# Optimization experiments

Hardware: AMD Instinct MI355X
Metric: run time of the kernel (lower is better)

The kernel has to match this reference:

```python
import jax, jax.numpy as jnp
import numpy as np

S = 4096
F = 512  # in_features, head_num == 1 so per-head dim == F


def setup_inputs() -> dict:
    key = jax.random.key(0)
    ks = jax.random.split(key, 11)
    std = 0.02
    inp = {
        "q": jax.random.normal(ks[0], (1, S, F), jnp.float32),
        "k": jax.random.normal(ks[1], (1, S, F), jnp.float32),
        "v": jax.random.normal(ks[2], (1, S, F), jnp.float32),
        "Wq": jax.random.normal(ks[3], (F, F), jnp.float32) * std,
        "bq": jax.random.normal(ks[4], (F,), jnp.float32) * std,
        "Wk": jax.random.normal(ks[5], (F, F), jnp.float32) * std,
        "bk": jax.random.normal(ks[6], (F,), jnp.float32) * std,
        "Wv": jax.random.normal(ks[7], (F, F), jnp.float32) * std,
        "bv": jax.random.normal(ks[8], (F,), jnp.float32) * std,
        "Wo": jax.random.normal(ks[9], (F, F), jnp.float32) * std,
        "bo": jax.random.normal(ks[10], (F,), jnp.float32) * std,
    }
    return inp


def reference(q, k, v, Wq, bq, Wk, bk, Wv, bv, Wo, bo):
    dk = Wq.shape[0]  # head_num == 1 -> per-head dim equals in_features
    # q_k, q_v: projections of q WITHOUT activation (as in original forward)
    q_k = q @ Wk.T + bk            # (1, S, F)
    q_v = q @ Wv.T + bv            # (1, S, F)
    # activated projections (F.relu)
    qq = jax.nn.relu(q @ Wq.T + bq)[0]  # (S, F)
    kk = jax.nn.relu(k @ Wk.T + bk)[0]  # (S, F)
    vv = jax.nn.relu(v @ Wv.T + bv)[0]  # (S, F)
    # diagonal of qq @ q_k^T, computed without materializing the SxS matrix
    q_att = jnp.sum(qq * q_k[0], axis=-1, keepdims=True)  # (S, 1)
    scores = jnp.einsum('sd,td->st', qq, kk)               # (S, S)
    scores = jnp.concatenate([scores, q_att], axis=-1)     # (S, S+1)
    scores = scores / np.sqrt(dk + 1).astype(np.float32)
    attn = jax.nn.softmax(scores, axis=-1)                 # (S, S+1)
    res = attn[:, :-1] @ vv                                # (S, F)
    res = q_v[0] * q_att + res                             # elementwise fusion
    y = res[None]                                          # (1, S, F)
    y = jax.nn.relu(y @ Wo.T + bo)
    return y
```

## Files before the change

kernel.cpp:

```cpp
#include <hip/hip_runtime.h>
#include <math.h>

#define S_LEN 4096
#define F_DIM 512
#define PSPLIT 8
#define FIXED_M 4.0f

typedef __attribute__((ext_vector_type(8))) short bf16x8;
typedef __attribute__((ext_vector_type(4))) float f32x4;

__device__ __forceinline__ unsigned short f2bf(float x) {
    union { float f; unsigned u; } v; v.f = x;
    unsigned r = v.u + 0x7fffu + ((v.u >> 16) & 1u);
    return (unsigned short)(r >> 16);
}
__device__ __forceinline__ float bf2f(unsigned short b) {
    union { unsigned u; float f; } v; v.u = ((unsigned)b) << 16;
    return v.f;
}
__device__ __forceinline__ void load_lds16(const void* g, void* l) {
    __builtin_amdgcn_global_load_lds(
        (const __attribute__((address_space(1))) unsigned int*)g,
        (__attribute__((address_space(3))) unsigned int*)l, 16, 0, 0);
}

struct CastArgs {
    const float* src[7];
    unsigned short* dst[7];
    int n4[7];
};
__global__ void cast_all(CastArgs a) {
    int r = blockIdx.y;
    int i = blockIdx.x * blockDim.x + threadIdx.x;
    if (i >= a.n4[r]) return;
    float4 v = ((const float4*)a.src[r])[i];
    ushort4 o;
    o.x = f2bf(v.x); o.y = f2bf(v.y); o.z = f2bf(v.z); o.w = f2bf(v.w);
    ((ushort4*)a.dst[r])[i] = o;
}

__global__ void transpose_bf16(const unsigned short* __restrict__ src,
                               unsigned short* __restrict__ dst) {
    __shared__ __align__(16) unsigned short tile[64][72];
    const int s0 = blockIdx.x * 64, f0 = blockIdx.y * 64;
    const int tid = threadIdx.x;
#pragma unroll
    for (int it = 0; it < 2; ++it) {
        int u = it * 256 + tid;
        int r = u >> 3, c = (u & 7) * 8;
        *(uint4*)&tile[r][c] = *(const uint4*)(src + (size_t)(s0 + r) * F_DIM + f0 + c);
    }
    __syncthreads();
#pragma unroll
    for (int it = 0; it < 2; ++it) {
        int u = it * 256 + tid;
        int fl = u >> 3, sc = (u & 7) * 8;
        unsigned short tmp[8];
#pragma unroll
        for (int i = 0; i < 8; ++i) tmp[i] = tile[sc + i][fl];
        *(uint4*)(dst + (size_t)(f0 + fl) * S_LEN + s0 + sc) = *(uint4*)tmp;
    }
}

#define GEMM_KLOOP(XPTR, LDX, WPTR, LDW, KBEG, KEND)                                  \
    for (int k0 = (KBEG); k0 < (KEND); k0 += 64) {                                    \
        __syncthreads();                                                              \
        _Pragma("unroll")                                                             \
        for (int i = 0; i < 2; ++i) {                                                 \
            int c = w * 2 + i;                                                        \
            _Pragma("unroll")                                                         \
            for (int kh = 0; kh < 2; ++kh) {                                          \
                load_lds16((XPTR) + (size_t)(m0 + c * 16 + ln) * (LDX) + k0 + kh * 32 + quad * 8, \
                           &As[(c * 2 + kh) * 512]);                                  \
                load_lds16((WPTR) + (size_t)(n0 + c * 16 + ln) * (LDW) + k0 + kh * 32 + quad * 8, \
                           &Bs[(c * 2 + kh) * 512]);                                  \
            }                                                                         \
        }                                                                             \
        __syncthreads();                                                              \
        _Pragma("unroll")                                                             \
        for (int kh = 0; kh < 2; ++kh) {                                              \
            bf16x8 af[4], bfr[4];                                                     \
            _Pragma("unroll")                                                         \
            for (int mt = 0; mt < 4; ++mt)                                            \
                af[mt] = *(const bf16x8*)&As[((wr * 4 + mt) * 2 + kh) * 512 + l * 8];  \
            _Pragma("unroll")                                                         \
            for (int nt = 0; nt < 4; ++nt)                                            \
                bfr[nt] = *(const bf16x8*)&Bs[((wc * 4 + nt) * 2 + kh) * 512 + l * 8]; \
            _Pragma("unroll")                                                         \
            for (int mt = 0; mt < 4; ++mt)                                            \
                _Pragma("unroll")                                                     \
                for (int nt = 0; nt < 4; ++nt)                                        \
                    acc[mt][nt] = __builtin_amdgcn_mfma_f32_16x16x32_bf16(            \
                        af[mt], bfr[nt], acc[mt][nt], 0, 0, 0);                       \
        }                                                                             \
    }

struct GemmDesc {
    const unsigned short* X;
    const unsigned short* W;
    const float* bias;
    unsigned short* out_bf;
    float* out_f32;
    int relu;
};
struct GemmArgs { GemmDesc d[5]; };

__launch_bounds__(256, 2)
__global__ void gemm128(GemmArgs args) {
    __shared__ __align__(16) unsigned short As[16 * 512];
    __shared__ __align__(16) unsigned short Bs[16 * 512];
    const GemmDesc d = args.d[blockIdx.y >> 2];
    const int n0 = (blockIdx.y & 3) * 128;
    const int m0 = blockIdx.x * 128;
    const int tid = threadIdx.x;
    const int w = tid >> 6, l = tid & 63, quad = l >> 4, ln = l & 15;
    const int wr = w >> 1, wc = w & 1;

    f32x4 acc[4][4];
    f32x4 zero4 = {0.f, 0.f, 0.f, 0.f};
#pragma unroll
    for (int i = 0; i < 4; ++i)
#pragma unroll
        for (int j = 0; j < 4; ++j) acc[i][j] = zero4;

    GEMM_KLOOP(d.X, F_DIM, d.W, F_DIM, 0, F_DIM)

#pragma unroll
    for (int mt = 0; mt < 4; ++mt)
#pragma unroll
        for (int nt = 0; nt < 4; ++nt)
#pragma unroll
            for (int r = 0; r < 4; ++r) {
                int row = m0 + wr * 64 + mt * 16 + quad * 4 + r;
                int col = n0 + wc * 64 + nt * 16 + ln;
                float vv = acc[mt][nt][r] + d.bias[col];
                if (d.relu) vv = fmaxf(vv, 0.f);
                if (d.out_bf)  d.out_bf[(size_t)row * F_DIM + col] = f2bf(vv);
                if (d.out_f32) d.out_f32[(size_t)row * F_DIM + col] = vv;
            }
}

__launch_bounds__(256, 2)
__global__ void gemm_exp(const unsigned short* __restrict__ X,
                         const unsigned short* __restrict__ W,
                         unsigned short* __restrict__ P,
                         float* __restrict__ lpart) {
    __shared__ __align__(16) unsigned short As[16 * 512];
    __shared__ __align__(16) unsigned short Bs[16 * 512];
    __shared__ float lsum[2][2][64];
    const float scale = 0.04415108f;
    const int nb = blockIdx.y;
    const int n0 = nb * 128;
    const int m0 = blockIdx.x * 128;
    const int tid = threadIdx.x;
    const int w = tid >> 6, l = tid & 63, quad = l >> 4, ln = l & 15;
    const int wr = w >> 1, wc = w & 1;

    f32x4 acc[4][4];
    f32x4 zero4 = {0.f, 0.f, 0.f, 0.f};
#pragma unroll
    for (int i = 0; i < 4; ++i)
#pragma unroll
        for (int j = 0; j < 4; ++j) acc[i][j] = zero4;

    GEMM_KLOOP(X, F_DIM, W, F_DIM, 0, F_DIM)

    float rs[4][4];
#pragma unroll
    for (int mt = 0; mt < 4; ++mt)
#pragma unroll
        for (int r = 0; r < 4; ++r) rs[mt][r] = 0.f;

#pragma unroll
    for (int mt = 0; mt < 4; ++mt)
#pragma unroll
        for (int nt = 0; nt < 4; ++nt)
#pragma unroll
            for (int r = 0; r < 4; ++r) {
                int row = m0 + wr * 64 + mt * 16 + quad * 4 + r;
                int col = n0 + wc * 64 + nt * 16 + ln;
                float p = __expf(acc[mt][nt][r] * scale - FIXED_M);
                P[(size_t)row * S_LEN + col] = f2bf(p);
                rs[mt][r] += p;
            }
#pragma unroll
    for (int mt = 0; mt < 4; ++mt)
#pragma unroll
        for (int r = 0; r < 4; ++r) {
            float v = rs[mt][r];
            v += __shfl_xor(v, 1);
            v += __shfl_xor(v, 2);
            v += __shfl_xor(v, 4);
            v += __shfl_xor(v, 8);
            if (ln == 0) lsum[wr][wc][mt * 16 + quad * 4 + r] = v;
        }
    __syncthreads();
    if (tid < 128)
        lpart[(size_t)nb * S_LEN + m0 + tid] =
            lsum[tid >> 6][0][tid & 63] + lsum[tid >> 6][1][tid & 63];
}

__launch_bounds__(256, 2)
__global__ void gemm_pv(const unsigned short* __restrict__ P,
                        const unsigned short* __restrict__ vt,
                        unsigned short* __restrict__ O_p) {
    __shared__ __align__(16) unsigned short As[16 * 512];
    __shared__ __align__(16) unsigned short Bs[16 * 512];
    const int nb = blockIdx.y & 3;
    const int split = blockIdx.y >> 2;
    const int n0 = nb * 128;
    const int m0 = blockIdx.x * 128;
    const int koff = split * (S_LEN / PSPLIT);
    const int tid = threadIdx.x;
    const int w = tid >> 6, l = tid & 63, quad = l >> 4, ln = l & 15;
    const int wr = w >> 1, wc = w & 1;

    f32x4 acc[4][4];
    f32x4 zero4 = {0.f, 0.f, 0.f, 0.f};
#pragma unroll
    for (int i = 0; i < 4; ++i)
#pragma unroll
        for (int j = 0; j < 4; ++j) acc[i][j] = zero4;

    GEMM_KLOOP(P, S_LEN, vt, S_LEN, koff, koff + S_LEN / PSPLIT)

    unsigned short* Op = O_p + (size_t)split * S_LEN * F_DIM;
#pragma unroll
    for (int mt = 0; mt < 4; ++mt)
#pragma unroll
        for (int nt = 0; nt < 4; ++nt)
#pragma unroll
            for (int r = 0; r < 4; ++r) {
                int row = m0 + wr * 64 + mt * 16 + quad * 4 + r;
                int col = n0 + wc * 64 + nt * 16 + ln;
                Op[(size_t)row * F_DIM + col] = f2bf(acc[mt][nt][r]);
            }
}

__global__ void combine_kernel(const unsigned short* __restrict__ O_p,
                               const float* __restrict__ lpart,
                               const unsigned short* __restrict__ qq,
                               const unsigned short* __restrict__ qk,
                               const unsigned short* __restrict__ qv,
                               unsigned short* __restrict__ res_bf) {
    const float scale = 0.04415108f;
    int row = blockIdx.x;
    int t = threadIdx.x;
    int wv = t >> 6, l = t & 63;
    __shared__ float wsum[2];

    ushort4 a = *(const ushort4*)(qq + (size_t)row * F_DIM + t * 4);
    ushort4 b = *(const ushort4*)(qk + (size_t)row * F_DIM + t * 4);
    float part = bf2f(a.x) * bf2f(b.x) + bf2f(a.y) * bf2f(b.y) +
                 bf2f(a.z) * bf2f(b.z) + bf2f(a.w) * bf2f(b.w);
#pragma unroll
    for (int off = 32; off >= 1; off >>= 1) part += __shfl_xor(part, off);
    if (l == 0) wsum[wv] = part;
    __syncthreads();
    float qa = wsum[0] + wsum[1];

    float denom = __expf(qa * scale - FIXED_M);
#pragma unroll
    for (int i = 0; i < 32; ++i) denom += lpart[(size_t)i * S_LEN + row];
    float inv = 1.f / denom;

    for (int f = t; f < F_DIM; f += 128) {
        float acc = 0.f;
#pragma unroll
        for (int i = 0; i < PSPLIT; ++i)
            acc += bf2f(O_p[((size_t)i * S_LEN + row) * F_DIM + f]);
        float r = bf2f(qv[(size_t)row * F_DIM + f]) * qa + acc * inv;
        res_bf[(size_t)row * F_DIM + f] = f2bf(r);
    }
}

extern "C" void kernel_launch(void* const* d_in, const int* in_sizes, int n_in,
                              void* d_out, int out_size, void* d_ws, size_t ws_size,
                              hipStream_t stream) {
    const float* q  = (const float*)d_in[0];
    const float* k  = (const float*)d_in[1];
    const float* v  = (const float*)d_in[2];
    const float* Wq = (const float*)d_in[3];
    const float* bq = (const float*)d_in[4];
    const float* Wk = (const float*)d_in[5];
    const float* bk = (const float*)d_in[6];
    const float* Wv = (const float*)d_in[7];
    const float* bv = (const float*)d_in[8];
    const float* Wo = (const float*)d_in[9];
    const float* bo = (const float*)d_in[10];
    float* out = (float*)d_out;

    char* p = (char*)d_ws;
    auto alloc = [&](size_t bytes) -> char* {
        char* r = p; p += (bytes + 255) & ~(size_t)255; return r;
    };
    const size_t SF = (size_t)S_LEN * F_DIM;
    unsigned short* q_bf  = (unsigned short*)alloc(SF * 2);
    unsigned short* k_bf  = (unsigned short*)alloc(SF * 2);
    unsigned short* v_bf  = (unsigned short*)alloc(SF * 2);
    unsigned short* qq_bf = (unsigned short*)alloc(SF * 2);
    unsigned short* kk_bf = (unsigned short*)alloc(SF * 2);
    unsigned short* vv_bf = (unsigned short*)alloc(SF * 2);
    unsigned short* vt_bf = (unsigned short*)alloc(SF * 2);
    unsigned short* qk_bf = (unsigned short*)alloc(SF * 2);
    unsigned short* qv_bf = (unsigned short*)alloc(SF * 2);
    unsigned short* res_bf = (unsigned short*)alloc(SF * 2);
    unsigned short* wq_bf = (unsigned short*)alloc((size_t)F_DIM * F_DIM * 2);
    unsigned short* wk_bf = (unsigned short*)alloc((size_t)F_DIM * F_DIM * 2);
    unsigned short* wv_bf = (unsigned short*)alloc((size_t)F_DIM * F_DIM * 2);
    unsigned short* wo_bf = (unsigned short*)alloc((size_t)F_DIM * F_DIM * 2);
    unsigned short* P_bf  = (unsigned short*)alloc((size_t)S_LEN * S_LEN * 2);
    float* lpart = (float*)alloc((size_t)32 * S_LEN * 4);
    unsigned short* O_p = (unsigned short*)alloc((size_t)PSPLIT * SF * 2);

    CastArgs ca;
    ca.src[0] = q;  ca.dst[0] = q_bf;  ca.n4[0] = (int)(SF / 4);
    ca.src[1] = k;  ca.dst[1] = k_bf;  ca.n4[1] = (int)(SF / 4);
    ca.src[2] = v;  ca.dst[2] = v_bf;  ca.n4[2] = (int)(SF / 4);
    ca.src[3] = Wq; ca.dst[3] = wq_bf; ca.n4[3] = F_DIM * F_DIM / 4;
    ca.src[4] = Wk; ca.dst[4] = wk_bf; ca.n4[4] = F_DIM * F_DIM / 4;
    ca.src[5] = Wv; ca.dst[5] = wv_bf; ca.n4[5] = F_DIM * F_DIM / 4;
    ca.src[6] = Wo; ca.dst[6] = wo_bf; ca.n4[6] = F_DIM * F_DIM / 4;
    cast_all<<<dim3((unsigned)(SF / 4 / 256), 7), 256, 0, stream>>>(ca);

    GemmArgs ga;
    ga.d[0] = { q_bf, wq_bf, bq, qq_bf, nullptr, 1 };
    ga.d[1] = { k_bf, wk_bf, bk, kk_bf, nullptr, 1 };
    ga.d[2] = { v_bf, wv_bf, bv, vv_bf, nullptr, 1 };
    ga.d[3] = { q_bf, wk_bf, bk, qk_bf, nullptr, 0 };
    ga.d[4] = { q_bf, wv_bf, bv, qv_bf, nullptr, 0 };
    gemm128<<<dim3(S_LEN / 128, 20), 256, 0, stream>>>(ga);

    transpose_bf16<<<dim3(S_LEN / 64, F_DIM / 64), 256, 0, stream>>>(vv_bf, vt_bf);

    gemm_exp<<<dim3(S_LEN / 128, S_LEN / 128), 256, 0, stream>>>(qq_bf, kk_bf, P_bf, lpart);

    gemm_pv<<<dim3(S_LEN / 128, 4 * PSPLIT), 256, 0, stream>>>(P_bf, vt_bf, O_p);

    combine_kernel<<<S_LEN, 128, 0, stream>>>(O_p, lpart, qq_bf, qk_bf, qv_bf, res_bf);

    GemmArgs ga2{};
    ga2.d[0] = { res_bf, wo_bf, bo, nullptr, out, 1 };
    gemm128<<<dim3(S_LEN / 128, 4), 256, 0, stream>>>(ga2);
}
```

Baseline: 245.3 us.

## Use 256x128 tiles for attention GEMMs and split-K the output projection

The QK^T+exp and PV kernels now use 256x128 block tiles: each wave computes 64x128 and reuses one shared B tile across all eight N-subtiles. This raises the MFMA-to-LDS-load ratio and halves the number of blocks, at the cost of more accumulator registers and more LDS. The row-sum reduction now writes partial sums straight from shuffles and no longer goes through shared memory. The final Wo projection, which launched only 128 blocks, is split into two K segments writing fp32 partials, followed by a small reduce kernel that adds bias and applies ReLU, to expose more parallelism.

```diff
diff --git a/kernel.cpp b/kernel.cpp
--- a/kernel.cpp
+++ b/kernel.cpp
@@ -95,6 +95,44 @@
         }                                                                             \
     }
 
+#define KLOOP256(XPTR, LDX, WPTR, LDW, KBEG, KEND)                                    \
+    for (int k0 = (KBEG); k0 < (KEND); k0 += 64) {                                    \
+        __syncthreads();                                                              \
+        _Pragma("unroll")                                                             \
+        for (int i = 0; i < 4; ++i) {                                                 \
+            int g = w * 4 + i;                                                        \
+            _Pragma("unroll")                                                         \
+            for (int kh = 0; kh < 2; ++kh)                                            \
+                load_lds16((XPTR) + (size_t)(m0 + g * 16 + ln) * (LDX) + k0 + kh * 32 + quad * 8, \
+                           &As[(g * 2 + kh) * 512]);                                  \
+        }                                                                             \
+        _Pragma("unroll")                                                             \
+        for (int i = 0; i < 2; ++i) {                                                 \
+            int g2 = w * 2 + i;                                                       \
+            _Pragma("unroll")                                                         \
+            for (int kh = 0; kh < 2; ++kh)                                            \
+                load_lds16((WPTR) + (size_t)(n0 + g2 * 16 + ln) * (LDW) + k0 + kh * 32 + quad * 8, \
+                           &Bs[(g2 * 2 + kh) * 512]);                                 \
+        }                                                                             \
+        __syncthreads();                                                              \
+        _Pragma("unroll")                                                             \
+        for (int kh = 0; kh < 2; ++kh) {                                              \
+            bf16x8 af[4], bfr[8];                                                     \
+            _Pragma("unroll")                                                         \
+            for (int mt = 0; mt < 4; ++mt)                                            \
+                af[mt] = *(const bf16x8*)&As[((w * 4 + mt) * 2 + kh) * 512 + l * 8];   \
+            _Pragma("unroll")                                                         \
+            for (int nt = 0; nt < 8; ++nt)                                            \
+                bfr[nt] = *(const bf16x8*)&Bs[(nt * 2 + kh) * 512 + l * 8];            \
+            _Pragma("unroll")                                                         \
+            for (int mt = 0; mt < 4; ++mt)                                            \
+                _Pragma("unroll")                                                     \
+                for (int nt = 0; nt < 8; ++nt)                                        \
+                    acc[mt][nt] = __builtin_amdgcn_mfma_f32_16x16x32_bf16(            \
+                        af[mt], bfr[nt], acc[mt][nt], 0, 0, 0);                       \
+        }                                                                             \
+    }
+
 struct GemmDesc {
     const unsigned short* X;
     const unsigned short* W;
@@ -145,11 +183,89 @@
                          const unsigned short* __restrict__ W,
                          unsigned short* __restrict__ P,
                          float* __restrict__ lpart) {
+    __shared__ __align__(16) unsigned short As[32 * 512];
+    __shared__ __align__(16) unsigned short Bs[16 * 512];
+    const float scale = 0.04415108f;
+    const int nb = blockIdx.y;
+    const int n0 = nb * 128;
+    const int m0 = blockIdx.x * 256;
+    const int tid = threadIdx.x;
+    const int w = tid >> 6, l = tid & 63, quad = l >> 4, ln = l & 15;
+
+    f32x4 acc[4][8];
+    f32x4 zero4 = {0.f, 0.f, 0.f, 0.f};
+#pragma unroll
+    for (int i = 0; i < 4; ++i)
+#pragma unroll
+        for (int j = 0; j < 8; ++j) acc[i][j] = zero4;
+
+    KLOOP256(X, F_DIM, W, F_DIM, 0, F_DIM)
+
+#pragma unroll
+    for (int mt = 0; mt < 4; ++mt)
+#pragma unroll
+        for (int r = 0; r < 4; ++r) {
+            int row = m0 + w * 64 + mt * 16 + quad * 4 + r;
+            float rs = 0.f;
+#pragma unroll
+            for (int nt = 0; nt < 8; ++nt) {
+                int col = n0 + nt * 16 + ln;
+                float p = __expf(acc[mt][nt][r] * scale - FIXED_M);
+                P[(size_t)row * S_LEN + col] = f2bf(p);
+                rs += p;
+            }
+            rs += __shfl_xor(rs, 1);
+            rs += __shfl_xor(rs, 2);
+            rs += __shfl_xor(rs, 4);
+            rs += __shfl_xor(rs, 8);
+            if (ln == 0) lpart[(size_t)nb * S_LEN + row] = rs;
+        }
+}
+
+__launch_bounds__(256, 2)
+__global__ void gemm_pv(const unsigned short* __restrict__ P,
+                        const unsigned short* __restrict__ vt,
+                        unsigned short* __restrict__ O_p) {
+    __shared__ __align__(16) unsigned short As[32 * 512];
+    __shared__ __align__(16) unsigned short Bs[16 * 512];
+    const int nb = blockIdx.y & 3;
+    const int split = blockIdx.y >> 2;
+    const int n0 = nb * 128;
+    const int m0 = blockIdx.x * 256;
+    const int koff = split * (S_LEN / PSPLIT);
+    const int tid = threadIdx.x;
+    const int w = tid >> 6, l = tid & 63, quad = l >> 4, ln = l & 15;
+
+    f32x4 acc[4][8];
+    f32x4 zero4 = {0.f, 0.f, 0.f, 0.f};
+#pragma unroll
+    for (int i = 0; i < 4; ++i)
+#pragma unroll
+        for (int j = 0; j < 8; ++j) acc[i][j] = zero4;
+
+    KLOOP256(P, S_LEN, vt, S_LEN, koff, koff + S_LEN / PSPLIT)
+
+    unsigned short* Op = O_p + (size_t)split * S_LEN * F_DIM;
+#pragma unroll
+    for (int mt = 0; mt < 4; ++mt)
+#pragma unroll
+        for (int nt = 0; nt < 8; ++nt)
+#pragma unroll
+            for (int r = 0; r < 4; ++r) {
+                int row = m0 + w * 64 + mt * 16 + quad * 4 + r;
+                int col = n0 + nt * 16 + ln;
+                Op[(size_t)row * F_DIM + col] = f2bf(acc[mt][nt][r]);
+            }
+}
+
+__launch_bounds__(256, 2)
+__global__ void gemm_final(const unsigned short* __restrict__ X,
+                           const unsigned short* __restrict__ W,
+                           float* __restrict__ Fp) {
     __shared__ __align__(16) unsigned short As[16 * 512];
     __shared__ __align__(16) unsigned short Bs[16 * 512];
-    __shared__ float lsum[2][2][64];
-    const float scale = 0.04415108f;
-    const int nb = blockIdx.y;
+    const int nb = blockIdx.y & 3;
+    const int kseg = blockIdx.y >> 2;
     const int n0 = nb * 128;
     const int m0 = blockIdx.x * 128;
     const int tid = threadIdx.x;
@@ -163,14 +279,9 @@
 #pragma unroll
         for (int j = 0; j < 4; ++j) acc[i][j] = zero4;
 
-    GEMM_KLOOP(X, F_DIM, W, F_DIM, 0, F_DIM)
-
-    float rs[4][4];
-#pragma unroll
-    for (int mt = 0; mt < 4; ++mt)
-#pragma unroll
-        for (int r = 0; r < 4; ++r) rs[mt][r] = 0.f;
-
+    GEMM_KLOOP(X, F_DIM, W, F_DIM, kseg * 256, kseg * 256 + 256)
+
+    float* Op = Fp + (size_t)kseg * S_LEN * F_DIM;
 #pragma unroll
     for (int mt = 0; mt < 4; ++mt)
 #pragma unroll
@@ -179,62 +290,24 @@
             for (int r = 0; r < 4; ++r) {
                 int row = m0 + wr * 64 + mt * 16 + quad * 4 + r;
                 int col = n0 + wc * 64 + nt * 16 + ln;
-                float p = __expf(acc[mt][nt][r] * scale - FIXED_M);
-                P[(size_t)row * S_LEN + col] = f2bf(p);
-                rs[mt][r] += p;
+                Op[(size_t)row * F_DIM + col] = acc[mt][nt][r];
             }
-#pragma unroll
-    for (int mt = 0; mt < 4; ++mt)
-#pragma unroll
-        for (int r = 0; r < 4; ++r) {
-            float v = rs[mt][r];
-            v += __shfl_xor(v, 1);
-            v += __shfl_xor(v, 2);
-            v += __shfl_xor(v, 4);
-            v += __shfl_xor(v, 8);
-            if (ln == 0) lsum[wr][wc][mt * 16 + quad * 4 + r] = v;
-        }
-    __syncthreads();
-    if (tid < 128)
-        lpart[(size_t)nb * S_LEN + m0 + tid] =
-            lsum[tid >> 6][0][tid & 63] + lsum[tid >> 6][1][tid & 63];
-}
-
-__launch_bounds__(256, 2)
-__global__ void gemm_pv(const unsigned short* __restrict__ P,
-                        const unsigned short* __restrict__ vt,
-                        unsigned short* __restrict__ O_p) {
-    __shared__ __align__(16) unsigned short As[16 * 512];
-    __shared__ __align__(16) unsigned short Bs[16 * 512];
-    const int nb = blockIdx.y & 3;
-    const int split = blockIdx.y >> 2;
-    const int n0 = nb * 128;
-    const int m0 = blockIdx.x * 128;
-    const int koff = split * (S_LEN / PSPLIT);
-    const int tid = threadIdx.x;
-    const int w = tid >> 6, l = tid & 63, quad = l >> 4, ln = l & 15;
-    const int wr = w >> 1, wc = w & 1;
-
-    f32x4 acc[4][4];
-    f32x4 zero4 = {0.f, 0.f, 0.f, 0.f};
-#pragma unroll
-    for (int i = 0; i < 4; ++i)
-#pragma unroll
-        for (int j = 0; j < 4; ++j) acc[i][j] = zero4;
-
-    GEMM_KLOOP(P, S_LEN, vt, S_LEN, koff, koff + S_LEN / PSPLIT)
-
-    unsigned short* Op = O_p + (size_t)split * S_LEN * F_DIM;
-#pragma unroll
-    for (int mt = 0; mt < 4; ++mt)
-#pragma unroll
-        for (int nt = 0; nt < 4; ++nt)
-#pragma unroll
-            for (int r = 0; r < 4; ++r) {
-                int row = m0 + wr * 64 + mt * 16 + quad * 4 + r;
-                int col = n0 + wc * 64 + nt * 16 + ln;
-                Op[(size_t)row * F_DIM + col] = f2bf(acc[mt][nt][r]);
-            }
+}
+
+__global__ void reduce_final(const float* __restrict__ Fp,
+                             const float* __restrict__ bias,
+                             float* __restrict__ out) {
+    int i = blockIdx.x * blockDim.x + threadIdx.x;
+    int col4 = (i & (F_DIM / 4 - 1)) * 4;
+    float4 a = ((const float4*)Fp)[i];
+    float4 b = ((const float4*)(Fp + (size_t)S_LEN * F_DIM))[i];
+    float4 bi = *(const float4*)(bias + col4);
+    float4 o;
+    o.x = fmaxf(a.x + b.x + bi.x, 0.f);
+    o.y = fmaxf(a.y + b.y + bi.y, 0.f);
+    o.z = fmaxf(a.z + b.z + bi.z, 0.f);
+    o.w = fmaxf(a.w + b.w + bi.w, 0.f);
+    ((float4*)out)[i] = o;
 }
 
 __global__ void combine_kernel(const unsigned short* __restrict__ O_p,
@@ -312,6 +385,7 @@
     unsigned short* P_bf  = (unsigned short*)alloc((size_t)S_LEN * S_LEN * 2);
     float* lpart = (float*)alloc((size_t)32 * S_LEN * 4);
     unsigned short* O_p = (unsigned short*)alloc((size_t)PSPLIT * SF * 2);
+    float* Fp = (float*)alloc((size_t)2 * SF * 4);
 
     CastArgs ca;
     ca.src[0] = q;  ca.dst[0] = q_bf;  ca.n4[0] = (int)(SF / 4);
@@ -333,13 +407,12 @@
 
     transpose_bf16<<<dim3(S_LEN / 64, F_DIM / 64), 256, 0, stream>>>(vv_bf, vt_bf);
 
-    gemm_exp<<<dim3(S_LEN / 128, S_LEN / 128), 256, 0, stream>>>(qq_bf, kk_bf, P_bf, lpart);
-
-    gemm_pv<<<dim3(S_LEN / 128, 4 * PSPLIT), 256, 0, stream>>>(P_bf, vt_bf, O_p);
+    gemm_exp<<<dim3(S_LEN / 256, S_LEN / 128), 256, 0, stream>>>(qq_bf, kk_bf, P_bf, lpart);
+
+    gemm_pv<<<dim3(S_LEN / 256, 4 * PSPLIT), 256, 0, stream>>>(P_bf, vt_bf, O_p);
 
     combine_kernel<<<S_LEN, 128, 0, stream>>>(O_p, lpart, qq_bf, qk_bf, qv_bf, res_bf);
 
-    GemmArgs ga2{};
-    ga2.d[0] = { res_bf, wo_bf, bo, nullptr, out, 1 };
-    gemm128<<<dim3(S_LEN / 128, 4), 256, 0, stream>>>(ga2);
-}
+    gemm_final<<<dim3(S_LEN / 128, 8), 256, 0, stream>>>(res_bf, wo_bf, Fp);
+    reduce_final<<<(unsigned)(SF / 4 / 256), 256, 0, stream>>>(Fp, bo, out);
+}
```

Measured after the change: 219.6 us, median of 2. 1.12x faster.
